# Kernel optimization log

Measured on AMD Instinct MI355X. Metric: run time of the kernel, lower is better.

## Reference

```python
import jax, jax.numpy as jnp
import numpy as np


def _lstm_layer(x, w_ih, w_hh, b, h0, c0):
    # x: [S, B, H]; w_ih, w_hh: [4H, H]; b: [4H] (b_ih + b_hh combined)
    H = h0.shape[-1]

    def step(carry, xt):
        h, c = carry
        gates = xt @ w_ih.T + h @ w_hh.T + b  # [B, 4H]
        i = jax.nn.sigmoid(gates[:, 0 * H:1 * H])
        f = jax.nn.sigmoid(gates[:, 1 * H:2 * H])
        g = jnp.tanh(gates[:, 2 * H:3 * H])
        o = jax.nn.sigmoid(gates[:, 3 * H:4 * H])
        c = f * c + i * g
        h = o * jnp.tanh(c)
        return (h, c), h

    (_, _), hs = jax.lax.scan(step, (h0, c0), x)
    return hs  # [S, B, H]


def setup_inputs() -> dict:
    key = jax.random.key(0)
    ks = jax.random.split(key, 5)
    S, B, H, L, C = 256, 64, 1024, 2, 10
    return {
        "x_data": jax.random.normal(ks[0], (S, B, H), dtype=jnp.float32),
        "weight": jax.random.normal(ks[1], (L, 2, 4 * H, H), dtype=jnp.float32) * 0.05,
        "bias": jax.random.normal(ks[2], (L, 2, 4 * H), dtype=jnp.float32) * 0.05,
        "fc_w": jax.random.normal(ks[3], (C, H), dtype=jnp.float32) * 0.05,
        "fc_b": jax.random.normal(ks[4], (C,), dtype=jnp.float32) * 0.05,
        "hiddenSize": H,
        "miniBatch": B,
        "seqLength": S,
        "numLayers": L,
    }


def reference(x_data, weight, bias, fc_w, fc_b, hiddenSize, miniBatch, seqLength, numLayers):
    B, H = miniBatch, hiddenSize
    h0 = jnp.zeros((B, H), dtype=x_data.dtype)
    c0 = jnp.zeros((B, H), dtype=x_data.dtype)
    x = x_data
    for layer in range(numLayers):
        w_ih = weight[layer, 0]  # [4H, H]
        w_hh = weight[layer, 1]  # [4H, H]
        b = bias[layer, 0] + bias[layer, 1]  # [4H]
        x = _lstm_layer(x, w_ih, w_hh, b, h0, c0)
    out = x[-1]  # last timestep of top layer: [B, H]
    return out @ fc_w.T + fc_b  # [B, num_classes]
```

## Files before the change

kernel.cpp:

```cpp
#include <hip/hip_runtime.h>
#include <cstdint>
#include <cstddef>

#define S_LEN 256
#define BATCH 64
#define HID   1024
#define GATES 4096
#define NBLK  256
#define RING_D 4
#define FLAG_STRIDE 32

typedef _Float16 h16;
typedef _Float16 h16x8 __attribute__((ext_vector_type(8)));
typedef _Float16 h16x4 __attribute__((ext_vector_type(4)));
typedef float    f32x4 __attribute__((ext_vector_type(4)));

__global__ __launch_bounds__(256)
void xconv_kernel(const float* __restrict__ x, h16* __restrict__ x16)
{
  const int n4 = S_LEN * BATCH * HID / 4;
  const int stride = gridDim.x * 256;
  for (int i = blockIdx.x * 256 + threadIdx.x; i < n4; i += stride) {
    f32x4 v = ((const f32x4*)x)[i];
    h16x4 o;
    o[0] = (h16)v[0]; o[1] = (h16)v[1]; o[2] = (h16)v[2]; o[3] = (h16)v[3];
    ((h16x4*)x16)[i] = o;
  }
}

#define RLOAD(dst, ptr, OFFSTR)                                         \
  asm volatile("global_load_dwordx4 %0, %1, off offset:" OFFSTR " sc1"  \
               : "=&v"(dst) : "v"(ptr) : "memory")

__global__ __launch_bounds__(512, 1)
void lstm_persistent(const h16* __restrict__ x16,
                     const float* __restrict__ weight,
                     const float* __restrict__ bias,
                     h16* __restrict__ h0r,
                     h16* __restrict__ h1r,
                     unsigned* __restrict__ flags)
{
  __shared__ h16   wlds[65536];
  __shared__ float plds[8][16][32];

  const int wg    = blockIdx.x;
  const int layer = wg >> 7;
  const int j0    = (wg & 127) * 8;
  const int tid   = threadIdx.x;
  const int wave  = tid >> 6, lane = tid & 63;
  const int l15   = lane & 15, l16 = lane >> 4;
  const int BH    = BATCH * HID;

  {
    const float* wsrc = weight + (size_t)layer * 2 * GATES * HID;
    for (int c = tid; c < 8192; c += 512) {
      const int ln = c & 63, s = (c >> 6) & 7, n2 = (c >> 9) & 1, w = c >> 10;
      const int lc  = n2 * 16 + (ln & 15);
      const int col = (lc >> 3) * HID + j0 + (lc & 7);
      const int k   = w * 256 + s * 32 + (ln >> 4) * 8;
      const float* p = wsrc + (k < HID ? (size_t)0 : (size_t)GATES * HID)
                            + (size_t)col * HID + (k & (HID - 1));
      h16x8 v;
#pragma unroll
      for (int e = 0; e < 8; ++e) v[e] = (h16)p[e];
      *(h16x8*)&wlds[(size_t)c * 8] = v;
    }
  }
  float bc[4];
  {
    const int j = tid & 7;
#pragma unroll
    for (int gg = 0; gg < 4; ++gg) {
      const int col = gg * HID + j0 + j;
      bc[gg] = bias[(size_t)layer * 2 * GATES + col] +
               bias[(size_t)layer * 2 * GATES + GATES + col];
    }
  }
  float creg[4] = {0.f, 0.f, 0.f, 0.f};
  __syncthreads();

  const int own_base = layer * 128;
  const int oth_base = (1 - layer) * 128;

  for (int t = 0; t < S_LEN; ++t) {
    {
      if (tid < 128) {
        const unsigned tg = (unsigned)t;
        if (tg)
          while (__hip_atomic_load(&flags[(own_base + tid) * FLAG_STRIDE],
                                   __ATOMIC_RELAXED,
                                   __HIP_MEMORY_SCOPE_AGENT) < tg) {}
      } else if (tid < 256) {
        const int ct = layer ? (t + 1) : (t + 1 - RING_D);
        if (ct > 0) {
          const unsigned tg = (unsigned)ct;
          while (__hip_atomic_load(&flags[(oth_base + tid - 128) * FLAG_STRIDE],
                                   __ATOMIC_RELAXED,
                                   __HIP_MEMORY_SCOPE_AGENT) < tg) {}
        }
      }
      __syncthreads();
    }

    const h16 *Alo, *Ahi;
    h16* Hout;
    if (layer == 0) {
      Alo  = x16 + (size_t)t * BH;
      Ahi  = h0r + (size_t)((t + RING_D - 1) % RING_D) * BH;
      Hout = h0r + (size_t)(t % RING_D) * BH;
    } else {
      Alo  = h0r + (size_t)(t % RING_D) * BH;
      Ahi  = h1r + (size_t)((t + 1) & 1) * BH;
      Hout = h1r + (size_t)(t & 1) * BH;
    }
    const h16* Asrc = (wave < 4) ? Alo : Ahi;
    const bool ring = (layer == 1) || (wave >= 4);
    const int kb = (wave & 3) * 256;

    const h16* arow[4];
#pragma unroll
    for (int i = 0; i < 4; ++i)
      arow[i] = Asrc + (size_t)(i * 16 + l15) * HID + kb + l16 * 8;
    const h16* bb = wlds + (size_t)wave * 8192 + lane * 8;

    h16x8 a[8][4];
    if (ring) {
#pragma unroll
      for (int i = 0; i < 4; ++i) {
        RLOAD(a[0][i], arow[i], "0");
        RLOAD(a[1][i], arow[i], "64");
        RLOAD(a[2][i], arow[i], "128");
        RLOAD(a[3][i], arow[i], "192");
        RLOAD(a[4][i], arow[i], "256");
        RLOAD(a[5][i], arow[i], "320");
        RLOAD(a[6][i], arow[i], "384");
        RLOAD(a[7][i], arow[i], "448");
      }
      asm volatile("s_waitcnt vmcnt(0)" ::: "memory");
      __builtin_amdgcn_sched_barrier(0);
    } else {
#pragma unroll
      for (int s = 0; s < 8; ++s)
#pragma unroll
        for (int i = 0; i < 4; ++i)
          a[s][i] = *(const h16x8*)(arow[i] + s * 32);
    }

    f32x4 acc[4][2];
#pragma unroll
    for (int i = 0; i < 4; ++i)
#pragma unroll
      for (int n2 = 0; n2 < 2; ++n2) acc[i][n2] = (f32x4)0.f;

#pragma unroll
    for (int s = 0; s < 8; ++s) {
      const h16x8 b0 = *(const h16x8*)(bb + s * 512);
      const h16x8 b1 = *(const h16x8*)(bb + 4096 + s * 512);
#pragma unroll
      for (int i = 0; i < 4; ++i) {
        acc[i][0] = __builtin_amdgcn_mfma_f32_16x16x32_f16(a[s][i], b0, acc[i][0], 0, 0, 0);
        acc[i][1] = __builtin_amdgcn_mfma_f32_16x16x32_f16(a[s][i], b1, acc[i][1], 0, 0, 0);
      }
    }

#pragma unroll
    for (int i = 0; i < 4; ++i) {
#pragma unroll
      for (int n2 = 0; n2 < 2; ++n2)
#pragma unroll
        for (int q = 0; q < 4; ++q) {
          const int r = l16 * 4 + q;
          const int colS = (n2 * 16 + l15) ^ ((r & 7) << 2);
          plds[wave][r][colS] = acc[i][n2][q];
        }
      __syncthreads();
      if (tid < 128) {
        const int r = tid >> 3, j = tid & 7;
        float gv[4];
#pragma unroll
        for (int gg = 0; gg < 4; ++gg) {
          const int colS = (gg * 8 + j) ^ ((r & 7) << 2);
          float s = bc[gg];
#pragma unroll
          for (int w = 0; w < 8; ++w) s += plds[w][r][colS];
          gv[gg] = s;
        }
        const float ig = 1.f / (1.f + __expf(-gv[0]));
        const float fg = 1.f / (1.f + __expf(-gv[1]));
        const float gt = 1.f - 2.f / (__expf(2.f * gv[2]) + 1.f);
        const float og = 1.f / (1.f + __expf(-gv[3]));
        const float cn = fg * creg[i] + ig * gt;
        creg[i] = cn;
        const float th = 1.f - 2.f / (__expf(2.f * cn) + 1.f);
        union { h16 f; unsigned short u; } hb;
        hb.f = (h16)(og * th);
        __hip_atomic_store(
            (unsigned short*)&Hout[(size_t)(i * 16 + r) * HID + j0 + j],
            hb.u, __ATOMIC_RELAXED, __HIP_MEMORY_SCOPE_AGENT);
      }
      __syncthreads();
    }

    if (tid == 0)
      __hip_atomic_store(&flags[wg * FLAG_STRIDE], (unsigned)(t + 1),
                         __ATOMIC_RELAXED, __HIP_MEMORY_SCOPE_AGENT);
  }
}

__global__ __launch_bounds__(256)
void fc_kernel(const h16* __restrict__ h,
               const float* __restrict__ fw,
               const float* __restrict__ fb,
               float* __restrict__ out)
{
  const int gw = (blockIdx.x * blockDim.x + threadIdx.x) >> 6;
  const int lane = threadIdx.x & 63;
  if (gw >= BATCH * 10) return;
  const int m = gw / 10, cls = gw % 10;
  float s = 0.f;
  for (int k = lane; k < HID; k += 64)
    s += (float)h[(size_t)m * HID + k] * fw[(size_t)cls * HID + k];
#pragma unroll
  for (int off = 32; off; off >>= 1) s += __shfl_down(s, off);
  if (lane == 0) out[m * 10 + cls] = s + fb[cls];
}

extern "C" void kernel_launch(void* const* d_in, const int* in_sizes, int n_in,
                              void* d_out, int out_size, void* d_ws, size_t ws_size,
                              hipStream_t stream)
{
  const float* x      = (const float*)d_in[0];
  const float* weight = (const float*)d_in[1];
  const float* bias   = (const float*)d_in[2];
  const float* fc_w   = (const float*)d_in[3];
  const float* fc_b   = (const float*)d_in[4];
  float* out = (float*)d_out;

  auto align = [](size_t v) { return (v + 255) & ~(size_t)255; };
  const size_t flags_sz = (size_t)NBLK * FLAG_STRIDE * sizeof(unsigned);
  const size_t x16_sz   = (size_t)S_LEN * BATCH * HID * sizeof(h16);
  const size_t h0r_sz   = (size_t)RING_D * BATCH * HID * sizeof(h16);
  const size_t h1r_sz   = (size_t)2 * BATCH * HID * sizeof(h16);

  char* p = (char*)d_ws;
  unsigned* flags = (unsigned*)p; p += align(flags_sz);
  h16* x16 = (h16*)p; p += align(x16_sz);
  h16* h0r = (h16*)p; p += align(h0r_sz);
  h16* h1r = (h16*)p; p += align(h1r_sz);

  hipMemsetAsync(flags, 0, flags_sz, stream);
  hipMemsetAsync(h0r, 0, h0r_sz, stream);
  hipMemsetAsync(h1r, 0, h1r_sz, stream);

  xconv_kernel<<<dim3(2048), 256, 0, stream>>>(x, x16);

  lstm_persistent<<<dim3(NBLK), dim3(512), 0, stream>>>(
      x16, weight, bias, h0r, h1r, flags);

  fc_kernel<<<dim3((BATCH * 10 * 64) / 256), 256, 0, stream>>>(
      h1r + (size_t)BATCH * HID, fc_w, fc_b, out);
}
```

Before: 2.900 ms.

## Split input and recurrent GEMM halves so input projection overlaps barrier wait

Each wave now covers a 128-wide K slice of both the input projection and the recurrent projection, where before waves were split between the two. The input-projection MFMAs run before the block waits on the own-layer flags, so that work is taken off the serial recurrent critical path and overlaps with the spin-wait. The cost is a reordered LDS weight layout and the layer-1 input loads going through the cache-bypassing path in two chunks. The recurrent part still needs a full sync per step.

New measurement: 2.702 ms. 6.8% less time.

```diff
diff --git a/kernel.cpp b/kernel.cpp
--- a/kernel.cpp
+++ b/kernel.cpp
@@ -54,12 +54,13 @@
   {
     const float* wsrc = weight + (size_t)layer * 2 * GATES * HID;
     for (int c = tid; c < 8192; c += 512) {
-      const int ln = c & 63, s = (c >> 6) & 7, n2 = (c >> 9) & 1, w = c >> 10;
+      const int ln = c & 63, s = (c >> 6) & 3, n2 = (c >> 8) & 1,
+                w = (c >> 9) & 7, part = c >> 12;
       const int lc  = n2 * 16 + (ln & 15);
       const int col = (lc >> 3) * HID + j0 + (lc & 7);
-      const int k   = w * 256 + s * 32 + (ln >> 4) * 8;
-      const float* p = wsrc + (k < HID ? (size_t)0 : (size_t)GATES * HID)
-                            + (size_t)col * HID + (k & (HID - 1));
+      const int k   = w * 128 + s * 32 + (ln >> 4) * 8;
+      const float* p = wsrc + (part ? (size_t)GATES * HID : (size_t)0)
+                            + (size_t)col * HID + k;
       h16x8 v;
 #pragma unroll
       for (int e = 0; e < 8; ++e) v[e] = (h16)p[e];
@@ -81,85 +82,118 @@
 
   const int own_base = layer * 128;
   const int oth_base = (1 - layer) * 128;
+  const h16* bbI = wlds + (size_t)wave * 4096 + lane * 8;
+  const h16* bbH = bbI + 32768;
+  const int kw = wave * 128 + l16 * 8;
 
   for (int t = 0; t < S_LEN; ++t) {
-    {
-      if (tid < 128) {
+    const h16* As;
+    if (layer == 0) {
+      As = x16 + (size_t)t * BH;
+    } else {
+      if (tid >= 128 && tid < 256) {
+        const unsigned tg = (unsigned)(t + 1);
+        while (__hip_atomic_load(&flags[(oth_base + tid - 128) * FLAG_STRIDE],
+                                 __ATOMIC_RELAXED,
+                                 __HIP_MEMORY_SCOPE_AGENT) < tg) {}
+      }
+      __syncthreads();
+      As = h0r + (size_t)(t % RING_D) * BH;
+    }
+
+    f32x4 accI[4][2];
+#pragma unroll
+    for (int i = 0; i < 4; ++i)
+#pragma unroll
+      for (int n2 = 0; n2 < 2; ++n2) accI[i][n2] = (f32x4)0.f;
+
+#pragma unroll
+    for (int sc = 0; sc < 2; ++sc) {
+      h16x8 aS[2][4];
+      if (layer == 0) {
+#pragma unroll
+        for (int ss = 0; ss < 2; ++ss)
+#pragma unroll
+          for (int i = 0; i < 4; ++i)
+            aS[ss][i] = *(const h16x8*)(As + (size_t)(i * 16 + l15) * HID +
+                                        kw + (sc * 2 + ss) * 32);
+      } else {
+#pragma unroll
+        for (int i = 0; i < 4; ++i) {
+          const h16* ap = As + (size_t)(i * 16 + l15) * HID + kw + sc * 64;
+          RLOAD(aS[0][i], ap, "0");
+          RLOAD(aS[1][i], ap, "64");
+        }
+        asm volatile("s_waitcnt vmcnt(0)" ::: "memory");
+        __builtin_amdgcn_sched_barrier(0);
+      }
+#pragma unroll
+      for (int ss = 0; ss < 2; ++ss) {
+        const int s = sc * 2 + ss;
+        const h16x8 b0 = *(const h16x8*)(bbI + s * 512);
+        const h16x8 b1 = *(const h16x8*)(bbI + 2048 + s * 512);
+#pragma unroll
+        for (int i = 0; i < 4; ++i) {
+          accI[i][0] = __builtin_amdgcn_mfma_f32_16x16x32_f16(aS[ss][i], b0, accI[i][0], 0, 0, 0);
+          accI[i][1] = __builtin_amdgcn_mfma_f32_16x16x32_f16(aS[ss][i], b1, accI[i][1], 0, 0, 0);
+        }
+      }
+    }
+
+    if (tid < 128) {
+      if (t) {
         const unsigned tg = (unsigned)t;
-        if (tg)
-          while (__hip_atomic_load(&flags[(own_base + tid) * FLAG_STRIDE],
-                                   __ATOMIC_RELAXED,
-                                   __HIP_MEMORY_SCOPE_AGENT) < tg) {}
-      } else if (tid < 256) {
-        const int ct = layer ? (t + 1) : (t + 1 - RING_D);
-        if (ct > 0) {
-          const unsigned tg = (unsigned)ct;
-          while (__hip_atomic_load(&flags[(oth_base + tid - 128) * FLAG_STRIDE],
-                                   __ATOMIC_RELAXED,
-                                   __HIP_MEMORY_SCOPE_AGENT) < tg) {}
-        }
-      }
-      __syncthreads();
-    }
-
-    const h16 *Alo, *Ahi;
+        while (__hip_atomic_load(&flags[(own_base + tid) * FLAG_STRIDE],
+                                 __ATOMIC_RELAXED,
+                                 __HIP_MEMORY_SCOPE_AGENT) < tg) {}
+      }
+    } else if (tid < 256 && layer == 0) {
+      const int ct = t + 1 - RING_D;
+      if (ct > 0) {
+        const unsigned tg = (unsigned)ct;
+        while (__hip_atomic_load(&flags[(oth_base + tid - 128) * FLAG_STRIDE],
+                                 __ATOMIC_RELAXED,
+                                 __HIP_MEMORY_SCOPE_AGENT) < tg) {}
+      }
+    }
+    __syncthreads();
+
+    const h16* Ah;
     h16* Hout;
     if (layer == 0) {
-      Alo  = x16 + (size_t)t * BH;
-      Ahi  = h0r + (size_t)((t + RING_D - 1) % RING_D) * BH;
+      Ah   = h0r + (size_t)((t + RING_D - 1) % RING_D) * BH;
       Hout = h0r + (size_t)(t % RING_D) * BH;
     } else {
-      Alo  = h0r + (size_t)(t % RING_D) * BH;
-      Ahi  = h1r + (size_t)((t + 1) & 1) * BH;
+      Ah   = h1r + (size_t)((t + 1) & 1) * BH;
       Hout = h1r + (size_t)(t & 1) * BH;
     }
-    const h16* Asrc = (wave < 4) ? Alo : Ahi;
-    const bool ring = (layer == 1) || (wave >= 4);
-    const int kb = (wave & 3) * 256;
-
-    const h16* arow[4];
+
+    h16x8 aH[4][4];
+#pragma unroll
+    for (int i = 0; i < 4; ++i) {
+      const h16* ap = Ah + (size_t)(i * 16 + l15) * HID + kw;
+      RLOAD(aH[i][0], ap, "0");
+      RLOAD(aH[i][1], ap, "64");
+      RLOAD(aH[i][2], ap, "128");
+      RLOAD(aH[i][3], ap, "192");
+    }
+    asm volatile("s_waitcnt vmcnt(0)" ::: "memory");
+    __builtin_amdgcn_sched_barrier(0);
+
+    f32x4 acc[4][2];
 #pragma unroll
     for (int i = 0; i < 4; ++i)
-      arow[i] = Asrc + (size_t)(i * 16 + l15) * HID + kb + l16 * 8;
-    const h16* bb = wlds + (size_t)wave * 8192 + lane * 8;
-
-    h16x8 a[8][4];
-    if (ring) {
+#pragma unroll
+      for (int n2 = 0; n2 < 2; ++n2) acc[i][n2] = accI[i][n2];
+
+#pragma unroll
+    for (int s = 0; s < 4; ++s) {
+      const h16x8 b0 = *(const h16x8*)(bbH + s * 512);
+      const h16x8 b1 = *(const h16x8*)(bbH + 2048 + s * 512);
 #pragma unroll
       for (int i = 0; i < 4; ++i) {
-        RLOAD(a[0][i], arow[i], "0");
-        RLOAD(a[1][i], arow[i], "64");
-        RLOAD(a[2][i], arow[i], "128");
-        RLOAD(a[3][i], arow[i], "192");
-        RLOAD(a[4][i], arow[i], "256");
-        RLOAD(a[5][i], arow[i], "320");
-        RLOAD(a[6][i], arow[i], "384");
-        RLOAD(a[7][i], arow[i], "448");
-      }
-      asm volatile("s_waitcnt vmcnt(0)" ::: "memory");
-      __builtin_amdgcn_sched_barrier(0);
-    } else {
-#pragma unroll
-      for (int s = 0; s < 8; ++s)
-#pragma unroll
-        for (int i = 0; i < 4; ++i)
-          a[s][i] = *(const h16x8*)(arow[i] + s * 32);
-    }
-
-    f32x4 acc[4][2];
-#pragma unroll
-    for (int i = 0; i < 4; ++i)
-#pragma unroll
-      for (int n2 = 0; n2 < 2; ++n2) acc[i][n2] = (f32x4)0.f;
-
-#pragma unroll
-    for (int s = 0; s < 8; ++s) {
-      const h16x8 b0 = *(const h16x8*)(bb + s * 512);
-      const h16x8 b1 = *(const h16x8*)(bb + 4096 + s * 512);
-#pragma unroll
-      for (int i = 0; i < 4; ++i) {
-        acc[i][0] = __builtin_amdgcn_mfma_f32_16x16x32_f16(a[s][i], b0, acc[i][0], 0, 0, 0);
-        acc[i][1] = __builtin_amdgcn_mfma_f32_16x16x32_f16(a[s][i], b1, acc[i][1], 0, 0, 0);
+        acc[i][0] = __builtin_amdgcn_mfma_f32_16x16x32_f16(aH[i][s], b0, acc[i][0], 0, 0, 0);
+        acc[i][1] = __builtin_amdgcn_mfma_f32_16x16x32_f16(aH[i][s], b1, acc[i][1], 0, 0, 0);
       }
     }
 
```
